# Kernel tuning notes

Measured on AMD Instinct MI355X. Metric: run time of the kernel, lower is better.

The kernel has to match this reference:

```python
import jax, jax.numpy as jnp
import numpy as np

T, D, K = 8192, 1024, 1024
LMBDA = 5.0
BIG = jnp.float32(3.0e38)  # finite stand-in for +inf so (f - lmbda) stays finite


def setup_inputs() -> dict:
    key = jax.random.key(0)
    k1, k2 = jax.random.split(key)
    return {
        "features": jax.random.normal(k1, (T, D), dtype=jnp.float32),
        "codebook": jax.random.normal(k2, (K, D), dtype=jnp.float32),
    }


def _dpdp(features, codebook, lmbda):
    # squared euclidean distances, (T, K)
    d2 = (
        jnp.sum(features * features, axis=1, keepdims=True)
        - 2.0 * features @ codebook.T
        + jnp.sum(codebook * codebook, axis=1)
    )
    Tn = features.shape[0]
    Kn = codebook.shape[0]

    # Incremental O(T*K) form of the original O(T^2*K) recurrence:
    # f_t[k] = min_{s<=t-1} alpha[s] - lmbda*(t-1-s) + sum_{i=s..t-1} d2[i,k]
    #        = d2[t-1,k] + min(alpha[t-1], f_{t-1}[k] - lmbda)
    # alpha[t] = min_k f_t[k]; beta[t] = start index s of argmin; gamma[t] = argmin_k.
    def fwd_step(carry, inp):
        f, s, alpha = carry  # f:(K,), s:(K,) segment start per codeword, alpha: scalar
        d_t, t = inp
        ext = f - lmbda                      # extend existing segment
        take_new = alpha < ext               # start a new segment at t
        f_new = d_t + jnp.minimum(alpha, ext)
        s_new = jnp.where(take_new, t, s)
        k_star = jnp.argmin(f_new)
        alpha_new = f_new[k_star]
        return (f_new, s_new, alpha_new), (s_new[k_star], k_star.astype(jnp.int32))

    init = (jnp.full((Kn,), BIG, jnp.float32), jnp.zeros((Kn,), jnp.int32), jnp.float32(0.0))
    ts = jnp.arange(Tn, dtype=jnp.int32)
    _, (betas, gammas) = jax.lax.scan(fwd_step, init, (d2, ts))
    # betas[t-1]/gammas[t-1] correspond to alpha index t in the original code.

    # Backtrack: units[beta[cur]:cur] = gamma[cur]; cur = beta[cur].
    def bwd_step(cur, p):
        g = gammas[cur - 1]
        b = betas[cur - 1]
        cur_new = jnp.where(p == b, p, cur)
        return cur_new, g

    _, units = jax.lax.scan(bwd_step, jnp.int32(Tn), ts, reverse=True)
    return units


def reference(features, codebook):
    units = _dpdp(features, codebook, LMBDA)
    quantized = codebook[units]
    quantized_st = features - jax.lax.stop_gradient(features - quantized)
    return quantized_st, units
```

## Files before the change

### kernel.cpp

```cpp
#include <hip/hip_runtime.h>
#include <hip/hip_bf16.h>
#include <stdint.h>

#define T_N 8192
#define K_N 1024
#define D_N 1024
#define LMBDA 5.0f
#define BIGF 3.0e38f
#define CMAX 32
#define THR 26.0f
#define QNAN 0x7FC00000

__global__ __launch_bounds__(256) void k_norms(const float* __restrict__ F,
                                               const float* __restrict__ C,
                                               float* __restrict__ sf2,
                                               float* __restrict__ sc2) {
#pragma clang fp contract(off)
  int wave = threadIdx.x >> 6;
  int lane = threadIdx.x & 63;
  int row = blockIdx.x * 4 + wave;
  const float* src;
  float* dst;
  if (row < T_N) { src = F + (size_t)row * D_N; dst = sf2 + row; }
  else           { src = C + (size_t)(row - T_N) * D_N; dst = sc2 + (row - T_N); }
  int leaf = lane >> 3, j = lane & 7;
  const float* p = src + leaf * 128 + j;
  float x = p[0];
  float r = x * x;
#pragma unroll
  for (int i = 1; i < 16; ++i) {
    float y = p[8 * i];
    r = r + y * y;
  }
  r = r + __shfl_xor(r, 1, 64);
  r = r + __shfl_xor(r, 2, 64);
  r = r + __shfl_xor(r, 4, 64);
  r = r + __shfl_xor(r, 8, 64);
  r = r + __shfl_xor(r, 16, 64);
  r = r + __shfl_xor(r, 32, 64);
  if (lane == 0) *dst = r;
}

__global__ __launch_bounds__(256) void k_gemm(const float* __restrict__ F,
                                              const float* __restrict__ C,
                                              const float* __restrict__ sf2,
                                              const float* __restrict__ sc2,
                                              float* __restrict__ d2) {
  __shared__ float As[32][68];
  __shared__ float Bs[32][132];
  int t0 = (int)(blockIdx.x >> 3) * 64;
  int k0 = (int)(blockIdx.x & 7) * 128;
  int tid = threadIdx.x;
  int tx = tid & 15, ty = tid >> 4;
  float dot[4][8], acc[4][8];
#pragma unroll
  for (int i = 0; i < 4; ++i)
#pragma unroll
    for (int j = 0; j < 8; ++j) { dot[i][j] = 0.0f; acc[i][j] = 0.0f; }
  int ra = tid & 63, ca = (tid >> 6) * 8;
  int rb = tid & 127, cb = (tid >> 7) * 16;
  for (int d0 = 0; d0 < D_N; d0 += 32) {
    __syncthreads();
    {
      const float* fa = &F[(size_t)(t0 + ra) * D_N + d0 + ca];
      float4 a0 = *(const float4*)fa;
      float4 a1 = *(const float4*)(fa + 4);
      As[ca + 0][ra] = a0.x; As[ca + 1][ra] = a0.y; As[ca + 2][ra] = a0.z; As[ca + 3][ra] = a0.w;
      As[ca + 4][ra] = a1.x; As[ca + 5][ra] = a1.y; As[ca + 6][ra] = a1.z; As[ca + 7][ra] = a1.w;
      const float* fb = &C[(size_t)(k0 + rb) * D_N + d0 + cb];
      float4 b0 = *(const float4*)fb;
      float4 b1 = *(const float4*)(fb + 4);
      float4 b2 = *(const float4*)(fb + 8);
      float4 b3 = *(const float4*)(fb + 12);
      Bs[cb + 0][rb] = b0.x; Bs[cb + 1][rb] = b0.y; Bs[cb + 2][rb] = b0.z; Bs[cb + 3][rb] = b0.w;
      Bs[cb + 4][rb] = b1.x; Bs[cb + 5][rb] = b1.y; Bs[cb + 6][rb] = b1.z; Bs[cb + 7][rb] = b1.w;
      Bs[cb + 8][rb] = b2.x; Bs[cb + 9][rb] = b2.y; Bs[cb + 10][rb] = b2.z; Bs[cb + 11][rb] = b2.w;
      Bs[cb + 12][rb] = b3.x; Bs[cb + 13][rb] = b3.y; Bs[cb + 14][rb] = b3.z; Bs[cb + 15][rb] = b3.w;
    }
    __syncthreads();
#pragma unroll
    for (int d = 0; d < 32; ++d) {
      float4 a = *(const float4*)&As[d][ty * 4];
      float4 b0 = *(const float4*)&Bs[d][tx * 4];
      float4 b1 = *(const float4*)&Bs[d][64 + tx * 4];
      float av[4] = {a.x, a.y, a.z, a.w};
      float bv[8] = {b0.x, b0.y, b0.z, b0.w, b1.x, b1.y, b1.z, b1.w};
#pragma unroll
      for (int i = 0; i < 4; ++i)
#pragma unroll
        for (int j = 0; j < 8; ++j)
          acc[i][j] = fmaf(av[i], bv[j], acc[i][j]);
    }
    if (d0 == 352) {
#pragma unroll
      for (int i = 0; i < 4; ++i)
#pragma unroll
        for (int j = 0; j < 8; ++j) { dot[i][j] = acc[i][j]; acc[i][j] = 0.0f; }
    }
    if (d0 == 736) {
#pragma unroll
      for (int i = 0; i < 4; ++i)
#pragma unroll
        for (int j = 0; j < 8; ++j) { dot[i][j] = dot[i][j] + acc[i][j]; acc[i][j] = 0.0f; }
    }
  }
  {
#pragma clang fp contract(off)
#pragma unroll
    for (int i = 0; i < 4; ++i) {
      int t = t0 + ty * 4 + i;
      float sa = sf2[t];
      float o[8];
#pragma unroll
      for (int j = 0; j < 4; ++j) {
        float dsum = dot[i][j] + acc[i][j];
        float two = 2.0f * dsum;
        o[j] = (sa - two) + sc2[k0 + tx * 4 + j];
      }
#pragma unroll
      for (int j = 4; j < 8; ++j) {
        float dsum = dot[i][j] + acc[i][j];
        float two = 2.0f * dsum;
        o[j] = (sa - two) + sc2[k0 + 64 + tx * 4 + (j - 4)];
      }
      float4 o0; o0.x = o[0]; o0.y = o[1]; o0.z = o[2]; o0.w = o[3];
      float4 o1; o1.x = o[4]; o1.y = o[5]; o1.z = o[6]; o1.w = o[7];
      float* dp = &d2[(size_t)t * K_N + k0 + tx * 4];
      *(float4*)dp = o0;
      *(float4*)(dp + 64) = o1;
    }
  }
}

__global__ __launch_bounds__(256) void k_cand(const float* __restrict__ d2,
                                              int2* __restrict__ cand,
                                              float* __restrict__ dminOut) {
  int wave = threadIdx.x >> 6;
  int lane = threadIdx.x & 63;
  int row = blockIdx.x * 4 + wave;
  const float4* p = (const float4*)(d2 + (size_t)row * K_N + lane * 16);
  float4 v0 = p[0], v1 = p[1], v2 = p[2], v3 = p[3];
  float m = fminf(fminf(fminf(v0.x, v0.y), fminf(v0.z, v0.w)),
                  fminf(fminf(v1.x, v1.y), fminf(v1.z, v1.w)));
  float n = fminf(fminf(fminf(v2.x, v2.y), fminf(v2.z, v2.w)),
                  fminf(fminf(v3.x, v3.y), fminf(v3.z, v3.w)));
  m = fminf(m, n);
  m = fminf(m, __shfl_xor(m, 1, 64));
  m = fminf(m, __shfl_xor(m, 2, 64));
  m = fminf(m, __shfl_xor(m, 4, 64));
  m = fminf(m, __shfl_xor(m, 8, 64));
  m = fminf(m, __shfl_xor(m, 16, 64));
  m = fminf(m, __shfl_xor(m, 32, 64));
  if (lane == 0) dminOut[row] = m;
  float thr = m + THR;
  unsigned flags = 0;
#define TESTC(J, VAL) if ((VAL) <= thr) flags |= (1u << (J));
  TESTC(0, v0.x) TESTC(1, v0.y) TESTC(2, v0.z) TESTC(3, v0.w)
  TESTC(4, v1.x) TESTC(5, v1.y) TESTC(6, v1.z) TESTC(7, v1.w)
  TESTC(8, v2.x) TESTC(9, v2.y) TESTC(10, v2.z) TESTC(11, v2.w)
  TESTC(12, v3.x) TESTC(13, v3.y) TESTC(14, v3.z) TESTC(15, v3.w)
#undef TESTC
  int c = __popc(flags);
  int pre = c;
#pragma unroll
  for (int off = 1; off <= 32; off <<= 1) {
    int t = __shfl_up(pre, off, 64);
    if (lane >= off) pre += t;
  }
  int idx = pre - c;
  int2* rowp = cand + (size_t)row * CMAX;
  int kb = lane * 16;
#define EMITC(J, VAL)                                                        \
  if (flags & (1u << (J))) {                                                 \
    if (idx < CMAX) rowp[idx] = make_int2(kb + (J), __float_as_int(VAL));    \
    ++idx;                                                                   \
  }
  EMITC(0, v0.x) EMITC(1, v0.y) EMITC(2, v0.z) EMITC(3, v0.w)
  EMITC(4, v1.x) EMITC(5, v1.y) EMITC(6, v1.z) EMITC(7, v1.w)
  EMITC(8, v2.x) EMITC(9, v2.y) EMITC(10, v2.z) EMITC(11, v2.w)
  EMITC(12, v3.x) EMITC(13, v3.y) EMITC(14, v3.z) EMITC(15, v3.w)
#undef EMITC
}

__global__ __launch_bounds__(256) void k_prev2(const int2* __restrict__ cand,
                                               int4* __restrict__ pairbuf) {
  __shared__ int km1k[4][32];
  __shared__ int km1d[4][32];
  __shared__ int kt0k[4][32];
  __shared__ int kt0d[4][32];
  int w = threadIdx.x >> 6, lane = threadIdx.x & 63;
  int p = blockIdx.x * 4 + w;
  int t0 = 2 * p, t1 = 2 * p + 1, tm1 = t0 - 1;
  if (lane < 32) {
    int2 c0 = cand[(size_t)t0 * CMAX + lane];
    kt0k[w][lane] = c0.x; kt0d[w][lane] = c0.y;
  } else {
    int j = lane - 32;
    int2 cm = (p > 0) ? cand[(size_t)tm1 * CMAX + j] : make_int2(-2, 0);
    km1k[w][j] = cm.x; km1d[w][j] = cm.y;
  }
  __syncthreads();
  int4 out;
  if (lane < 32) {
    int2 c1 = cand[(size_t)t1 * CMAX + lane];
    int k1 = c1.x;
    int pp2 = -4, d0 = QNAN, d1s = 0;
    bool in0 = false;
#pragma unroll
    for (int i = 0; i < 32; ++i) if (kt0k[w][i] == k1) { d0 = kt0d[w][i]; in0 = true; }
#pragma unroll
    for (int i = 0; i < 32; ++i) if (km1k[w][i] == k1) { pp2 = i * 4; d1s = km1d[w][i]; }
    if (!in0 || k1 < 0) { pp2 = -4; d0 = QNAN; }
    out = make_int4(pp2, d0, d1s, 0);
  } else {
    int i0 = lane - 32;
    int k0 = kt0k[w][i0];
    int d0 = kt0d[w][i0];
    int pp = -4, d1s = 0;
#pragma unroll
    for (int i = 0; i < 32; ++i) if (km1k[w][i] == k0) { pp = i * 4; d1s = km1d[w][i]; }
    if (k0 < 0) pp = -4;
    out = make_int4(pp, d0, d1s, 0);
  }
  pairbuf[(size_t)p * 64 + lane] = out;
}

__device__ __forceinline__ float dpp_min32(float x) {
  int t;
  t = __builtin_amdgcn_update_dpp(__float_as_int(x), __float_as_int(x), 0x111, 0xF, 0xF, false);
  x = fminf(x, __int_as_float(t));
  t = __builtin_amdgcn_update_dpp(__float_as_int(x), __float_as_int(x), 0x112, 0xF, 0xF, false);
  x = fminf(x, __int_as_float(t));
  t = __builtin_amdgcn_update_dpp(__float_as_int(x), __float_as_int(x), 0x114, 0xF, 0xF, false);
  x = fminf(x, __int_as_float(t));
  t = __builtin_amdgcn_update_dpp(__float_as_int(x), __float_as_int(x), 0x118, 0xF, 0xF, false);
  x = fminf(x, __int_as_float(t));
  t = __builtin_amdgcn_update_dpp(__float_as_int(x), __float_as_int(x), 0x142, 0xF, 0xF, false);
  x = fminf(x, __int_as_float(t));
  return x;
}
__device__ __forceinline__ float rdlane(float x, int l) {
  return __int_as_float(__builtin_amdgcn_readlane(__float_as_int(x), l));
}

__global__ __launch_bounds__(64, 1) void k_pass1(const int4* __restrict__ pairbuf,
                                                 const int2* __restrict__ cand,
                                                 const float* __restrict__ dminArr,
                                                 float* __restrict__ alphaOut) {
  const int lane = threadIdx.x;
  const int4* basep = pairbuf + lane;
  const int2* basec = cand + (lane & 31);
  int4 rg[8];
  int2 rgc[8];
#pragma unroll
  for (int u = 0; u < 8; ++u) {
    rg[u] = basep[(size_t)u * 64];
    rgc[u] = basec[(size_t)(2 * u + 1) * CMAX];
  }
  float mabprev = BIGF;
  float alpha = 0.0f;
  float redAB = 0.0f;
  float dmT1prev = 0.0f;
  float areg = 0.0f;
  float dmv_next = dminArr[lane];
  const int NP = T_N / 2;
  for (int pb32 = 0; pb32 < NP; pb32 += 32) {
    float dmv = dmv_next;
    int nb = pb32 + 32; if (nb >= NP) nb = 0;
    dmv_next = dminArr[2 * nb + lane];
    for (int pb8 = 0; pb8 < 32; pb8 += 8) {
#pragma unroll
      for (int u = 0; u < 8; ++u) {
        int p = pb32 + pb8 + u;
        int4 pv = rg[u];
        int2 cv = rgc[u];
        float aEnter = alpha;
        int g1 = __builtin_amdgcn_ds_bpermute(pv.x, __float_as_int(mabprev));
        int pn = p + 8; if (pn > NP - 1) pn = NP - 1;
        rg[u] = basep[(size_t)pn * 64];
        rgc[u] = basec[(size_t)(2 * pn + 1) * CMAX];
        float Pab = rdlane(redAB, 31);
        alpha = fminf(Pab, dmT1prev + aEnter);
        int posA = 2 * p - 1;
        if (posA >= 0) {
          areg = ((posA & 63) == lane) ? alpha : areg;
          if ((posA & 63) == 63) alphaOut[(posA & ~63) + lane] = areg;
        }
        int r0 = 2 * (pb8 + u);
        float dm0 = rdlane(dmv, r0);
        float dm1 = rdlane(dmv, r0 + 1);
        float inj = __int_as_float(pv.z) + aEnter;
        float fp = (pv.x < 0) ? BIGF : fminf(__int_as_float(g1), inj);
        float d0 = __int_as_float(pv.y);
        float d1 = __int_as_float(cv.y);
        float v0 = d0 + (fp - LMBDA);
        float A1 = d1 + (v0 - LMBDA);
        float B0 = d0 + alpha;
        float B1 = d1 + (B0 - LMBDA);
        float mab = fminf(A1, B1);
        float x = (lane < 32) ? mab : v0;
        float red = dpp_min32(x);
        float Pp0 = rdlane(red, 63);
        float a0 = fminf(Pp0, dm0 + alpha);
        areg = (((2 * p) & 63) == lane) ? a0 : areg;
        mabprev = mab;
        redAB = red;
        dmT1prev = dm1;
        alpha = a0;
      }
    }
  }
  float Pab = rdlane(redAB, 31);
  alpha = fminf(Pab, dmT1prev + alpha);
  areg = (lane == 63) ? alpha : areg;
  alphaOut[(T_N - 64) + lane] = areg;
}

#define CH 128
#define WARM 64
__global__ __launch_bounds__(256) void k_pass2(const float* __restrict__ d2,
                                               const float* __restrict__ AOUT,
                                               unsigned* __restrict__ pack) {
  int kb = blockIdx.x & 3;
  int tc = blockIdx.x >> 2;
  int k = kb * 256 + threadIdx.x;
  int ts = tc * CH;
  int start = ts - WARM; if (start < 0) start = 0;
  int end = ts + CH;
  __shared__ float lal[CH + WARM + 1];
  for (int i = threadIdx.x; i < end - start + 1; i += 256) {
    int idx = start - 1 + i;
    lal[i] = (idx < 0) ? 0.0f : AOUT[idx];
  }
  __syncthreads();
  float f = BIGF;
  unsigned s = 0;
#pragma unroll 4
  for (int tau = start; tau < end; ++tau) {
    float a_in = lal[tau - start];
    float d = d2[(size_t)tau * K_N + k];
    float ext = f - LMBDA;
    if (a_in < ext) s = (unsigned)tau;
    f = d + fminf(a_in, ext);
    if (tau >= ts) {
      float a_out = lal[tau - start + 1];
      if (f == a_out) atomicMin(&pack[tau], ((unsigned)k << 13) | s);
    }
  }
}

__global__ __launch_bounds__(256) void k_backtrack(const unsigned* __restrict__ pack,
                                                   unsigned* __restrict__ unitsWs,
                                                   float* __restrict__ outUnits) {
  __shared__ unsigned lp[T_N];
  __shared__ unsigned long long msk[T_N / 64];
  int tid = threadIdx.x;
  for (int i = tid * 4; i < T_N; i += 1024) {
    *(uint4*)&lp[i] = *(const uint4*)&pack[i];
  }
  __syncthreads();
  if (tid < 64) {
    int lane = tid;
    int cur = T_N;
    for (int B = T_N - 64; B >= 0; B -= 64) {
      unsigned long long marks = 0ull;
      if (cur > B) {
        unsigned pk = lp[B + lane];
        int bv = (int)(pk & 8191u);
        unsigned long long run = __ballot(bv == B + lane);
        while (cur > B) {
          int L = cur - 1 - B;
          unsigned long long below = (L == 63) ? ~0ull : ((1ull << (L + 1)) - 1ull);
          unsigned long long nz = (~run) & below;
          if (nz == 0ull) { marks |= below; cur = B; break; }
          int j = 63 - __builtin_clzll(nz);
          marks |= below & ~((1ull << j) - 1ull);
          int nb = __builtin_amdgcn_readlane(bv, j);
          cur = nb;
          if (cur > B + j) cur = B + j;
        }
      }
      if (lane == 0) msk[B >> 6] = marks;
    }
  }
  __syncthreads();
  for (int p = tid; p < T_N; p += 256) {
    int w = p >> 6;
    unsigned long long m = msk[w] & (~0ull << (p & 63));
    while (m == 0ull) { ++w; m = msk[w]; }
    int idx = (w << 6) + (int)__builtin_ctzll(m);
    unsigned g = (lp[idx] >> 13) & 1023u;
    unitsWs[p] = g;
    outUnits[p] = (float)g;
  }
}

__global__ __launch_bounds__(256) void k_gather(const float* __restrict__ C,
                                                const unsigned* __restrict__ unitsWs,
                                                float* __restrict__ out) {
  int t = blockIdx.x;
  unsigned u = unitsWs[t] & 1023u;
  const float4* src = (const float4*)(C + (size_t)u * D_N);
  float4* dst = (float4*)(out + (size_t)t * D_N);
  dst[threadIdx.x] = src[threadIdx.x];
}

extern "C" void kernel_launch(void* const* d_in, const int* in_sizes, int n_in,
                              void* d_out, int out_size, void* d_ws, size_t ws_size,
                              hipStream_t stream) {
  const float* F = (const float*)d_in[0];
  const float* C = (const float*)d_in[1];
  float* out = (float*)d_out;
  float* d2 = out;
  float* outUnits = out + (size_t)T_N * D_N;
  char* ws = (char*)d_ws;
  float* alphaOut = (float*)(ws);
  unsigned* pack = (unsigned*)(ws + (32 << 10));
  unsigned* unitsWs = (unsigned*)(ws + (64 << 10));
  float* sf2 = (float*)(ws + (96 << 10));
  float* sc2 = (float*)(ws + (128 << 10));
  float* dminArr = (float*)(ws + (160 << 10));
  int2* cand = (int2*)(ws + (1 << 20));
  int4* pairbuf = (int4*)(ws + (3 << 20));

  k_norms<<<(T_N + K_N) / 4, 256, 0, stream>>>(F, C, sf2, sc2);
  hipMemsetAsync(pack, 0xFF, T_N * sizeof(unsigned), stream);
  hipMemsetAsync(cand, 0xFF, (size_t)T_N * CMAX * sizeof(int2), stream);
  k_gemm<<<(T_N / 64) * (K_N / 128), 256, 0, stream>>>(F, C, sf2, sc2, d2);
  k_cand<<<T_N / 4, 256, 0, stream>>>(d2, cand, dminArr);
  k_prev2<<<(T_N / 2) / 4, 256, 0, stream>>>(cand, pairbuf);
  k_pass1<<<1, 64, 0, stream>>>(pairbuf, cand, dminArr, alphaOut);
  k_pass2<<<(T_N / CH) * 4, 256, 0, stream>>>(d2, alphaOut, pack);
  k_backtrack<<<1, 256, 0, stream>>>(pack, unitsWs, outUnits);
  k_gather<<<T_N, 256, 0, stream>>>(C, unitsWs, out);
}
```

Before: 899.9 us.

## Process four timesteps per serial iteration with 16-candidate sparse DP

Cuts the per-row candidate list from 32 to 16 entries and restructures the serial alpha recurrence in k_pass1 to advance four timesteps per loop iteration instead of two. Each group of 16 lanes handles one of the four rows, so the dependent chain of cross-lane reductions and readlanes per timestep shrinks. The preprocessing kernel now precomputes matches across four consecutive rows. Fewer candidates per row raises the risk that the true minimum falls outside the sparse set, which would make the results inexact.

```diff
diff --git a/kernel.cpp b/kernel.cpp
--- a/kernel.cpp
+++ b/kernel.cpp
@@ -7,7 +7,7 @@
 #define D_N 1024
 #define LMBDA 5.0f
 #define BIGF 3.0e38f
-#define CMAX 32
+#define CMAX 16
 #define THR 26.0f
 #define QNAN 0x7FC00000
 
@@ -182,50 +182,38 @@
 #undef EMITC
 }
 
-__global__ __launch_bounds__(256) void k_prev2(const int2* __restrict__ cand,
-                                               int4* __restrict__ pairbuf) {
-  __shared__ int km1k[4][32];
-  __shared__ int km1d[4][32];
-  __shared__ int kt0k[4][32];
-  __shared__ int kt0d[4][32];
+__global__ __launch_bounds__(256) void k_prev4(const int2* __restrict__ cand,
+                                               int4* __restrict__ pb1,
+                                               int2* __restrict__ pb2) {
+  __shared__ int2 rows[4][5][16];
   int w = threadIdx.x >> 6, lane = threadIdx.x & 63;
-  int p = blockIdx.x * 4 + w;
-  int t0 = 2 * p, t1 = 2 * p + 1, tm1 = t0 - 1;
-  if (lane < 32) {
-    int2 c0 = cand[(size_t)t0 * CMAX + lane];
-    kt0k[w][lane] = c0.x; kt0d[w][lane] = c0.y;
-  } else {
-    int j = lane - 32;
-    int2 cm = (p > 0) ? cand[(size_t)tm1 * CMAX + j] : make_int2(-2, 0);
-    km1k[w][j] = cm.x; km1d[w][j] = cm.y;
+  int g = blockIdx.x * 4 + w;
+  int base = 4 * g - 1;
+  for (int i = lane; i < 80; i += 64) {
+    int rr = i >> 4, ss = i & 15;
+    int trow = base + rr;
+    rows[w][rr][ss] = (trow >= 0) ? cand[(size_t)trow * CMAX + ss] : make_int2(-2, 0);
   }
   __syncthreads();
-  int4 out;
-  if (lane < 32) {
-    int2 c1 = cand[(size_t)t1 * CMAX + lane];
-    int k1 = c1.x;
-    int pp2 = -4, d0 = QNAN, d1s = 0;
-    bool in0 = false;
-#pragma unroll
-    for (int i = 0; i < 32; ++i) if (kt0k[w][i] == k1) { d0 = kt0d[w][i]; in0 = true; }
-#pragma unroll
-    for (int i = 0; i < 32; ++i) if (km1k[w][i] == k1) { pp2 = i * 4; d1s = km1d[w][i]; }
-    if (!in0 || k1 < 0) { pp2 = -4; d0 = QNAN; }
-    out = make_int4(pp2, d0, d1s, 0);
-  } else {
-    int i0 = lane - 32;
-    int k0 = kt0k[w][i0];
-    int d0 = kt0d[w][i0];
-    int pp = -4, d1s = 0;
-#pragma unroll
-    for (int i = 0; i < 32; ++i) if (km1k[w][i] == k0) { pp = i * 4; d1s = km1d[w][i]; }
-    if (k0 < 0) pp = -4;
-    out = make_int4(pp, d0, d1s, 0);
-  }
-  pairbuf[(size_t)p * 64 + lane] = out;
-}
-
-__device__ __forceinline__ float dpp_min32(float x) {
+  int q = 3 - (lane >> 4);
+  int s = lane & 15;
+  int2 me = rows[w][1 + q][s];
+  int k = me.x;
+  int pp = -4, p3s = QNAN;
+  int d0s = QNAN, d1s = QNAN, d2s = QNAN;
+#pragma unroll
+  for (int i = 0; i < 16; ++i) {
+    if (rows[w][0][i].x == k) { pp = i * 4; p3s = rows[w][0][i].y; }
+    if (rows[w][1][i].x == k) d0s = rows[w][1][i].y;
+    if (rows[w][2][i].x == k) d1s = rows[w][2][i].y;
+    if (rows[w][3][i].x == k) d2s = rows[w][3][i].y;
+  }
+  if (k < 0) pp = -4;
+  pb1[(size_t)g * 64 + lane] = make_int4(pp, me.y, d0s, d1s);
+  pb2[(size_t)g * 64 + lane] = make_int2(d2s, p3s);
+}
+
+__device__ __forceinline__ float dpp_min16(float x) {
   int t;
   t = __builtin_amdgcn_update_dpp(__float_as_int(x), __float_as_int(x), 0x111, 0xF, 0xF, false);
   x = fminf(x, __int_as_float(t));
@@ -235,84 +223,101 @@
   x = fminf(x, __int_as_float(t));
   t = __builtin_amdgcn_update_dpp(__float_as_int(x), __float_as_int(x), 0x118, 0xF, 0xF, false);
   x = fminf(x, __int_as_float(t));
-  t = __builtin_amdgcn_update_dpp(__float_as_int(x), __float_as_int(x), 0x142, 0xF, 0xF, false);
-  x = fminf(x, __int_as_float(t));
   return x;
 }
 __device__ __forceinline__ float rdlane(float x, int l) {
   return __int_as_float(__builtin_amdgcn_readlane(__float_as_int(x), l));
 }
 
-__global__ __launch_bounds__(64, 1) void k_pass1(const int4* __restrict__ pairbuf,
-                                                 const int2* __restrict__ cand,
+__global__ __launch_bounds__(64, 1) void k_pass1(const int4* __restrict__ pb1,
+                                                 const int2* __restrict__ pb2,
                                                  const float* __restrict__ dminArr,
                                                  float* __restrict__ alphaOut) {
   const int lane = threadIdx.x;
-  const int4* basep = pairbuf + lane;
-  const int2* basec = cand + (lane & 31);
-  int4 rg[8];
-  int2 rgc[8];
-#pragma unroll
-  for (int u = 0; u < 8; ++u) {
-    rg[u] = basep[(size_t)u * 64];
-    rgc[u] = basec[(size_t)(2 * u + 1) * CMAX];
-  }
-  float mabprev = BIGF;
-  float alpha = 0.0f;
-  float redAB = 0.0f;
-  float dmT1prev = 0.0f;
+  const int q = 3 - (lane >> 4);
+  const int4* b1p = pb1 + lane;
+  const int2* b2p = pb2 + lane;
+  int4 r1[4];
+  int2 r2[4];
+#pragma unroll
+  for (int u = 0; u < 4; ++u) {
+    r1[u] = b1p[(size_t)u * 64];
+    r2[u] = b2p[(size_t)u * 64];
+  }
+  float pay = 0.0f;
+  float red2c = BIGF;
+  float dm2c = 0.0f, dm3c = 0.0f, a1c = 0.0f;
   float areg = 0.0f;
-  float dmv_next = dminArr[lane];
-  const int NP = T_N / 2;
-  for (int pb32 = 0; pb32 < NP; pb32 += 32) {
-    float dmv = dmv_next;
-    int nb = pb32 + 32; if (nb >= NP) nb = 0;
-    dmv_next = dminArr[2 * nb + lane];
-    for (int pb8 = 0; pb8 < 32; pb8 += 8) {
-#pragma unroll
-      for (int u = 0; u < 8; ++u) {
-        int p = pb32 + pb8 + u;
-        int4 pv = rg[u];
-        int2 cv = rgc[u];
-        float aEnter = alpha;
-        int g1 = __builtin_amdgcn_ds_bpermute(pv.x, __float_as_int(mabprev));
-        int pn = p + 8; if (pn > NP - 1) pn = NP - 1;
-        rg[u] = basep[(size_t)pn * 64];
-        rgc[u] = basec[(size_t)(2 * pn + 1) * CMAX];
-        float Pab = rdlane(redAB, 31);
-        alpha = fminf(Pab, dmT1prev + aEnter);
-        int posA = 2 * p - 1;
-        if (posA >= 0) {
-          areg = ((posA & 63) == lane) ? alpha : areg;
-          if ((posA & 63) == 63) alphaOut[(posA & ~63) + lane] = areg;
+  const int NG = T_N / 4;
+  float dmv = dminArr[lane];
+  float dmv_next;
+  for (int gb = 0; gb < NG; gb += 16) {
+    int nb = gb + 16; if (nb >= NG) nb = 0;
+    dmv_next = dminArr[nb * 4 + lane];
+    for (int g4 = 0; g4 < 16; g4 += 4) {
+#pragma unroll
+      for (int u = 0; u < 4; ++u) {
+        int g = gb + g4 + u;
+        int4 pa = r1[u];
+        int2 pb = r2[u];
+        int g1 = __builtin_amdgcn_ds_bpermute(pa.x, __float_as_int(pay));
+        int gn = g + 4; if (gn > NG - 1) gn = NG - 1;
+        r1[u] = b1p[(size_t)gn * 64];
+        r2[u] = b2p[(size_t)gn * 64];
+        float at2p = fminf(rdlane(red2c, 31), dm2c + a1c);
+        float ain = fminf(rdlane(red2c, 15), dm3c + at2p);
+        int posB = 4 * g - 1;
+        if (posB >= 0) {
+          areg = (((posB - 1) & 63) == lane) ? at2p : areg;
+          areg = ((posB & 63) == lane) ? ain : areg;
+          if ((posB & 63) == 63) alphaOut[(posB & ~63) + lane] = areg;
         }
-        int r0 = 2 * (pb8 + u);
+        int r0 = 4 * (g4 + u);
         float dm0 = rdlane(dmv, r0);
         float dm1 = rdlane(dmv, r0 + 1);
-        float inj = __int_as_float(pv.z) + aEnter;
-        float fp = (pv.x < 0) ? BIGF : fminf(__int_as_float(g1), inj);
-        float d0 = __int_as_float(pv.y);
-        float d1 = __int_as_float(cv.y);
-        float v0 = d0 + (fp - LMBDA);
-        float A1 = d1 + (v0 - LMBDA);
-        float B0 = d0 + alpha;
-        float B1 = d1 + (B0 - LMBDA);
-        float mab = fminf(A1, B1);
-        float x = (lane < 32) ? mab : v0;
-        float red = dpp_min32(x);
-        float Pp0 = rdlane(red, 63);
-        float a0 = fminf(Pp0, dm0 + alpha);
-        areg = (((2 * p) & 63) == lane) ? a0 : areg;
-        mabprev = mab;
-        redAB = red;
-        dmT1prev = dm1;
-        alpha = a0;
+        float dm2 = rdlane(dmv, r0 + 2);
+        float dm3 = rdlane(dmv, r0 + 3);
+        float injE = __int_as_float(pb.y) + at2p;
+        float fp = (pa.x < 0) ? BIGF : fminf(__int_as_float(g1), injE);
+        float dOwn = __int_as_float(pa.y);
+        float d0s = __int_as_float(pa.z);
+        float d1s = __int_as_float(pa.w);
+        float d2s = __int_as_float(pb.x);
+        float A0 = d0s + (fp - LMBDA);
+        float A1 = d1s + (A0 - LMBDA);
+        float A2 = d2s + (A1 - LMBDA);
+        float A3 = dOwn + (A2 - LMBDA);
+        float B0 = d0s + ain;
+        float B1 = d1s + (B0 - LMBDA);
+        float B2 = d2s + (B1 - LMBDA);
+        float B3 = dOwn + (B2 - LMBDA);
+        float xA = (q == 0) ? A0 : (q == 1) ? A1 : (q == 2) ? A2 : A3;
+        float xB = (q == 0) ? B0 : (q == 1) ? B1 : (q == 2) ? B2 : B3;
+        float xAB = fminf(xA, xB);
+        float red1 = dpp_min16(xAB);
+        float a0 = rdlane(red1, 63);
+        float a1 = fminf(rdlane(red1, 47), dm1 + a0);
+        areg = (((4 * g) & 63) == lane) ? a0 : areg;
+        areg = (((4 * g + 1) & 63) == lane) ? a1 : areg;
+        float cw1 = d1s + a0;
+        float cw2 = d2s + (cw1 - LMBDA);
+        float Cin = (q == 2) ? cw1 : cw2;
+        float Cterm = dOwn + (Cin - LMBDA);
+        float Dterm = dOwn + ((d2s + a1) - LMBDA);
+        Dterm = (q == 3) ? Dterm : __int_as_float(QNAN);
+        float xr = fminf(fminf(xAB, Cterm), Dterm);
+        float red2 = dpp_min16(xr);
+        pay = xr;
+        red2c = red2;
+        dm2c = dm2; dm3c = dm3; a1c = a1;
       }
     }
-  }
-  float Pab = rdlane(redAB, 31);
-  alpha = fminf(Pab, dmT1prev + alpha);
-  areg = (lane == 63) ? alpha : areg;
+    dmv = dmv_next;
+  }
+  float at2 = fminf(rdlane(red2c, 31), dm2c + a1c);
+  float at3 = fminf(rdlane(red2c, 15), dm3c + at2);
+  areg = ((8190 & 63) == lane) ? at2 : areg;
+  areg = ((8191 & 63) == lane) ? at3 : areg;
   alphaOut[(T_N - 64) + lane] = areg;
 }
 
@@ -421,15 +426,16 @@
   float* sc2 = (float*)(ws + (128 << 10));
   float* dminArr = (float*)(ws + (160 << 10));
   int2* cand = (int2*)(ws + (1 << 20));
-  int4* pairbuf = (int4*)(ws + (3 << 20));
+  int4* pb1 = (int4*)(ws + (3 << 20));
+  int2* pb2 = (int2*)(ws + (5 << 20));
 
   k_norms<<<(T_N + K_N) / 4, 256, 0, stream>>>(F, C, sf2, sc2);
   hipMemsetAsync(pack, 0xFF, T_N * sizeof(unsigned), stream);
   hipMemsetAsync(cand, 0xFF, (size_t)T_N * CMAX * sizeof(int2), stream);
   k_gemm<<<(T_N / 64) * (K_N / 128), 256, 0, stream>>>(F, C, sf2, sc2, d2);
   k_cand<<<T_N / 4, 256, 0, stream>>>(d2, cand, dminArr);
-  k_prev2<<<(T_N / 2) / 4, 256, 0, stream>>>(cand, pairbuf);
-  k_pass1<<<1, 64, 0, stream>>>(pairbuf, cand, dminArr, alphaOut);
+  k_prev4<<<(T_N / 4) / 4, 256, 0, stream>>>(cand, pb1, pb2);
+  k_pass1<<<1, 64, 0, stream>>>(pb1, pb2, dminArr, alphaOut);
   k_pass2<<<(T_N / CH) * 4, 256, 0, stream>>>(d2, alphaOut, pack);
   k_backtrack<<<1, 256, 0, stream>>>(pack, unitsWs, outUnits);
   k_gather<<<T_N, 256, 0, stream>>>(C, unitsWs, out);
```

After: 849.9 us. 1.06x faster.
